# Kernel optimization log

Measured on AMD Instinct MI355X. Metric: run time of the kernel, lower is better.

## Reference

```python
import jax, jax.numpy as jnp
import numpy as np

EMBED = 1024
HEADS = 16
HEAD_DIM = EMBED // HEADS
BASE = 10000.0


def _rope_cos_sin(seq_len, dim, dtype):
    inv_freq = 1.0 / (BASE ** (jnp.arange(0, dim, 2, dtype=jnp.float32) / dim))
    t = jnp.arange(seq_len, dtype=jnp.float32)
    freqs = jnp.einsum('i,j->ij', t, inv_freq)           # [S, dim/2]
    emb = jnp.concatenate([freqs, freqs], axis=-1)        # [S, dim]
    return jnp.cos(emb).astype(dtype), jnp.sin(emb).astype(dtype)


def _rotate_half(x):
    d = x.shape[-1] // 2
    return jnp.concatenate([-x[..., d:], x[..., :d]], axis=-1)


def setup_inputs() -> dict:
    key = jax.random.key(0)
    ks = jax.random.split(key, 7)
    B, S = 2, 2048
    scale = 0.02
    return {
        'query': jax.random.normal(ks[0], (B, S, EMBED), jnp.float32),
        'key': jax.random.normal(ks[1], (B, S, EMBED), jnp.float32),
        'value': jax.random.normal(ks[2], (B, S, EMBED), jnp.float32),
        'Wq': jax.random.normal(ks[3], (EMBED, EMBED), jnp.float32) * scale,
        'Wk': jax.random.normal(ks[4], (EMBED, EMBED), jnp.float32) * scale,
        'Wv': jax.random.normal(ks[5], (EMBED, EMBED), jnp.float32) * scale,
        'Wo': jax.random.normal(ks[6], (EMBED, EMBED), jnp.float32) * scale,
    }


def reference(query, key, value, Wq, Wk, Wv, Wo):
    B, Sq, _ = query.shape
    Sk = key.shape[1]
    # projections (bias-free Linear: x @ W^T; W sampled so use x @ W directly)
    q = (query @ Wq).reshape(B, Sq, HEADS, HEAD_DIM).transpose(0, 2, 1, 3)  # [B,H,Sq,Dh]
    k = (key @ Wk).reshape(B, Sk, HEADS, HEAD_DIM).transpose(0, 2, 1, 3)
    v = (value @ Wv).reshape(B, Sk, HEADS, HEAD_DIM).transpose(0, 2, 1, 3)
    # RoPE applied to q and k per-position
    cos_q, sin_q = _rope_cos_sin(Sq, HEAD_DIM, q.dtype)  # [Sq,Dh]
    cos_k, sin_k = _rope_cos_sin(Sk, HEAD_DIM, k.dtype)
    q = q * cos_q[None, None] + _rotate_half(q) * sin_q[None, None]
    k = k * cos_k[None, None] + _rotate_half(k) * sin_k[None, None]
    scores = jnp.einsum('bhqd,bhkd->bhqk', q, k) / jnp.sqrt(jnp.asarray(HEAD_DIM, q.dtype))
    probs = jax.nn.softmax(scores, axis=-1)
    out = jnp.einsum('bhqk,bhkd->bhqd', probs, v)
    out = out.transpose(0, 2, 1, 3).reshape(B, Sq, EMBED)
    return out @ Wo
```

## Files before the change

kernel.cpp:

```cpp
#include <hip/hip_runtime.h>
#include <hip/hip_bf16.h>


typedef unsigned short u16;
typedef unsigned int u32;
typedef __attribute__((ext_vector_type(8))) short short8;
typedef __attribute__((ext_vector_type(4))) float f32x4;

#define MFMA16(a, b, c) __builtin_amdgcn_mfma_f32_16x16x32_bf16((a), (b), (c), 0, 0, 0)

typedef __attribute__((address_space(3))) u16 lds_u16;
typedef __attribute__((address_space(1))) const u16 glb_u16;

__device__ __forceinline__ void gload16(const u16* g, u16* l) {
    __builtin_amdgcn_global_load_lds((glb_u16*)g, (lds_u16*)l, 16, 0, 0);
}

__device__ __forceinline__ u16 f2bf(float f) {
    __hip_bfloat16 h = __float2bfloat16(f);
    return *reinterpret_cast<u16*>(&h);
}
__device__ __forceinline__ float bf2f(u16 b) {
    __hip_bfloat16 h;
    *reinterpret_cast<u16*>(&h) = b;
    return __bfloat162float(h);
}

__global__ __launch_bounds__(256) void conv_x(const float* __restrict__ q,
                                              const float* __restrict__ k,
                                              const float* __restrict__ v,
                                              u16* __restrict__ X3) {
    int z = blockIdx.y;
    const float* src = (z == 0) ? q : (z == 1) ? k : v;
    int i = (blockIdx.x * 256 + threadIdx.x) * 4;
    float4 f = *reinterpret_cast<const float4*>(src + i);
    ushort4 o;
    o.x = f2bf(f.x); o.y = f2bf(f.y); o.z = f2bf(f.z); o.w = f2bf(f.w);
    *reinterpret_cast<ushort4*>(X3 + (size_t)z * 4194304 + i) = o;
}

__global__ __launch_bounds__(256) void transpose_w(const float* __restrict__ w0,
                                                   const float* __restrict__ w1,
                                                   const float* __restrict__ w2,
                                                   const float* __restrict__ w3,
                                                   u16* __restrict__ WT) {
    __shared__ float t[32][33];
    const float* Ws[4] = {w0, w1, w2, w3};
    const float* W = Ws[blockIdx.z];
    int n0 = blockIdx.x * 32, k0 = blockIdx.y * 32;
    int tx = threadIdx.x, ty = threadIdx.y;
    for (int r = 0; r < 4; r++) {
        int kk = ty + r * 8;
        t[kk][tx] = W[(k0 + kk) * 1024 + n0 + tx];
    }
    __syncthreads();
    u16* out = WT + (size_t)blockIdx.z * 1048576;
    for (int r = 0; r < 4; r++) {
        int nn = ty + r * 8;
        out[(n0 + nn) * 1024 + k0 + tx] = f2bf(t[tx][nn]);
    }
}

template <typename OutT>
__global__ __launch_bounds__(256) void gemm_bt(const u16* __restrict__ A,
                                               const u16* __restrict__ Bt,
                                               OutT* __restrict__ C,
                                               int M, int N, int K) {
    int z = blockIdx.z;
    A  += (size_t)z * M * K;
    Bt += (size_t)z * N * K;
    C  += (size_t)z * M * N;
    int m0 = blockIdx.y * 128, n0 = blockIdx.x * 128;
    __shared__ u16 As[128 * 32];
    __shared__ u16 Bs[128 * 32];
    int tid = threadIdx.x;
    int wave = tid >> 6, lane = tid & 63, quad = lane >> 4, l16 = lane & 15;
    int wm = (wave >> 1) * 64, wn = (wave & 1) * 64;
    f32x4 acc[4][4];
    for (int i = 0; i < 4; i++)
        for (int j = 0; j < 4; j++)
            for (int r = 0; r < 4; r++) acc[i][j][r] = 0.f;

    for (int k0 = 0; k0 < K; k0 += 32) {
        __syncthreads();
        for (int c = 0; c < 2; c++) {
            int e = (tid + c * 256) * 8;
            int row = e >> 5, col = e & 31;
            gload16(&A[(size_t)(m0 + row) * K + k0 + col], &As[e]);
            gload16(&Bt[(size_t)(n0 + row) * K + k0 + col], &Bs[e]);
        }
        __syncthreads();
        short8 af[4], bfr[4];
        for (int i = 0; i < 4; i++)
            af[i] = *reinterpret_cast<const short8*>(&As[(wm + i * 16 + l16) * 32 + quad * 8]);
        for (int j = 0; j < 4; j++)
            bfr[j] = *reinterpret_cast<const short8*>(&Bs[(wn + j * 16 + l16) * 32 + quad * 8]);
        for (int i = 0; i < 4; i++)
            for (int j = 0; j < 4; j++)
                acc[i][j] = MFMA16(af[i], bfr[j], acc[i][j]);
    }

    for (int i = 0; i < 4; i++) {
        for (int r = 0; r < 4; r++) {
            int m = m0 + wm + i * 16 + quad * 4 + r;
            for (int j = 0; j < 4; j++) {
                int n = n0 + wn + j * 16 + l16;
                float v = acc[i][j][r];
                if constexpr (sizeof(OutT) == 2)
                    C[(size_t)m * N + n] = (OutT)f2bf(v);
                else
                    C[(size_t)m * N + n] = (OutT)v;
            }
        }
    }
}

__global__ __launch_bounds__(256) void rope_pack(const u16* __restrict__ QKV,
                                                 u16* __restrict__ Qp,
                                                 u16* __restrict__ Kp) {
    int z = blockIdx.y;
    int gid = blockIdx.x * 256 + threadIdx.x;
    int row = gid >> 5;
    int d = gid & 31;
    int b = row >> 15;
    int rem = row & 32767;
    int s = rem >> 4;
    int h = rem & 15;
    const u16* src = QKV + (size_t)z * 4194304 + (size_t)row * 64;
    float x1 = bf2f(src[d]);
    float x2 = bf2f(src[d + 32]);
    float inv = powf(10000.f, -(float)d / 32.f);
    float fr = (float)s * inv;
    float c = cosf(fr), sn = sinf(fr);
    float o1 = x1 * c - x2 * sn;
    float o2 = x2 * c + x1 * sn;
    if (z == 0) { o1 *= 0.125f; o2 *= 0.125f; }
    u16* dst = ((z == 0) ? Qp : Kp) + (((size_t)(b * 16 + h)) * 2048 + s) * 64;
    dst[d] = f2bf(o1);
    dst[d + 32] = f2bf(o2);
}

__global__ __launch_bounds__(256) void v_transpose(const u16* __restrict__ Vsrc,
                                                   u16* __restrict__ Vt) {
    __shared__ u16 t[64 * 72];
    int s0 = blockIdx.x * 64, bh = blockIdx.y;
    int b = bh >> 4, h = bh & 15;
    int tid = threadIdx.x;
    int srow = tid >> 3, scol = (tid & 7) * 8;
    for (int c = 0; c < 2; c++) {
        int s = srow + c * 32;
        *reinterpret_cast<int4*>(&t[s * 72 + scol]) =
            *reinterpret_cast<const int4*>(&Vsrc[((size_t)(b * 2048 + s0 + s)) * 1024 + h * 64 + scol]);
    }
    __syncthreads();
    for (int c = 0; c < 2; c++) {
        int d = srow + c * 32;
        short8 o;
        for (int j = 0; j < 8; j++) o[j] = (short)t[(scol + j) * 72 + d];
        *reinterpret_cast<short8*>(&Vt[(size_t)bh * 131072 + (size_t)d * 2048 + s0 + scol]) = o;
    }
}

__global__ __launch_bounds__(256) void flash_attn(const u16* __restrict__ Qp,
                                                  const u16* __restrict__ Kp,
                                                  const u16* __restrict__ Vt_g,
                                                  u16* __restrict__ attn) {
    int q0 = blockIdx.x * 64, bh = blockIdx.y;
    const u16* Q = Qp + (size_t)bh * 131072;
    const u16* K = Kp + (size_t)bh * 131072;
    const u16* Vt = Vt_g + (size_t)bh * 131072;
    __shared__ u16 Ks[64 * 72];
    __shared__ u16 Vs[64 * 72];
    __shared__ u16 Ps[64 * 72];
    int tid = threadIdx.x, wave = tid >> 6, lane = tid & 63;
    int quad = lane >> 4, l16 = lane & 15;
    int srow = tid >> 3, scol = (tid & 7) * 8;

    short8 qf[2];
    for (int kk = 0; kk < 2; kk++)
        qf[kk] = *reinterpret_cast<const short8*>(
            &Q[(size_t)(q0 + wave * 16 + l16) * 64 + kk * 32 + quad * 8]);

    float psum = 0.f;
    f32x4 Oacc[4];
    for (int dt = 0; dt < 4; dt++)
        for (int r = 0; r < 4; r++) Oacc[dt][r] = 0.f;

    for (int kv0 = 0; kv0 < 2048; kv0 += 64) {
        __syncthreads();
        for (int c = 0; c < 2; c++) {
            int row = srow + c * 32;
            *reinterpret_cast<int4*>(&Ks[row * 72 + scol]) =
                *reinterpret_cast<const int4*>(&K[(size_t)(kv0 + row) * 64 + scol]);
            *reinterpret_cast<int4*>(&Vs[row * 72 + scol]) =
                *reinterpret_cast<const int4*>(&Vt[(size_t)row * 2048 + kv0 + scol]);
        }
        __syncthreads();

        f32x4 st[4];
        for (int nt = 0; nt < 4; nt++)
            for (int r = 0; r < 4; r++) st[nt][r] = 0.f;
        for (int kk = 0; kk < 2; kk++)
            for (int nt = 0; nt < 4; nt++) {
                short8 af = *reinterpret_cast<const short8*>(
                    &Ks[(nt * 16 + l16) * 72 + kk * 32 + quad * 8]);
                st[nt] = MFMA16(af, qf[kk], st[nt]);
            }

        for (int nt = 0; nt < 4; nt++) {
            float p0 = __expf(st[nt][0]);
            float p1 = __expf(st[nt][1]);
            float p2 = __expf(st[nt][2]);
            float p3 = __expf(st[nt][3]);
            psum += (p0 + p1) + (p2 + p3);
            uint2 w;
            w.x = (u32)f2bf(p0) | ((u32)f2bf(p1) << 16);
            w.y = (u32)f2bf(p2) | ((u32)f2bf(p3) << 16);
            *reinterpret_cast<uint2*>(&Ps[(wave * 16 + l16) * 72 + nt * 16 + quad * 4]) = w;
        }

        for (int kk = 0; kk < 2; kk++) {
            short8 pa = *reinterpret_cast<const short8*>(
                &Ps[(wave * 16 + l16) * 72 + kk * 32 + quad * 8]);
            for (int dt = 0; dt < 4; dt++) {
                short8 bv = *reinterpret_cast<const short8*>(
                    &Vs[(dt * 16 + l16) * 72 + kk * 32 + quad * 8]);
                Oacc[dt] = MFMA16(pa, bv, Oacc[dt]);
            }
        }
    }

    psum += __shfl_xor(psum, 16);
    psum += __shfl_xor(psum, 32);
    float linv[4];
    for (int r = 0; r < 4; r++)
        linv[r] = 1.f / __shfl(psum, quad * 4 + r);

    int b = bh >> 4, h = bh & 15;
    for (int dt = 0; dt < 4; dt++)
        for (int r = 0; r < 4; r++) {
            int s = q0 + wave * 16 + quad * 4 + r;
            attn[((size_t)(b * 2048 + s)) * 1024 + h * 64 + dt * 16 + l16] =
                f2bf(Oacc[dt][r] * linv[r]);
        }
}

extern "C" void kernel_launch(void* const* d_in, const int* in_sizes, int n_in,
                              void* d_out, int out_size, void* d_ws, size_t ws_size,
                              hipStream_t stream) {
    const float* q  = (const float*)d_in[0];
    const float* k  = (const float*)d_in[1];
    const float* v  = (const float*)d_in[2];
    const float* wq = (const float*)d_in[3];
    const float* wk = (const float*)d_in[4];
    const float* wv = (const float*)d_in[5];
    const float* wo = (const float*)d_in[6];

    u16* ws = (u16*)d_ws;
    u16* WT  = ws;
    u16* X3  = ws + (size_t)4 * 1048576;
    u16* QKV = X3 + (size_t)3 * 4194304;
    u16* Qp   = X3;
    u16* Kp   = X3 + (size_t)1 * 4194304;
    u16* Vt_g = X3 + (size_t)2 * 4194304;
    u16* attn = QKV;

    conv_x<<<dim3(4096, 3), 256, 0, stream>>>(q, k, v, X3);
    transpose_w<<<dim3(32, 32, 4), dim3(32, 8), 0, stream>>>(wq, wk, wv, wo, WT);
    gemm_bt<u16><<<dim3(8, 32, 3), 256, 0, stream>>>(X3, WT, QKV, 4096, 1024, 1024);
    rope_pack<<<dim3(8192, 2), 256, 0, stream>>>(QKV, Qp, Kp);
    v_transpose<<<dim3(32, 32), 256, 0, stream>>>(QKV + (size_t)2 * 4194304, Vt_g);
    flash_attn<<<dim3(32, 32), 256, 0, stream>>>(Qp, Kp, Vt_g, attn);
    gemm_bt<float><<<dim3(8, 32, 1), 256, 0, stream>>>(
        attn, WT + (size_t)3 * 1048576, (float*)d_out, 4096, 1024, 1024);
}
```

Before: 285.9 us.

## Fuse RoPE into QKV GEMM epilogue and double query rows per attention block

The QKV projection epilogue now applies RoPE (from a precomputed cos/sin table) and the query scale, and writes head-major Q/K/V directly, so the separate rope_pack pass and its extra round trip through memory are gone. The RoPE table is built by a small kernel in the output buffer before the final GEMM overwrites it. Flash attention now processes 128 query rows per block (two 16-row groups per wave), so each K/V tile loaded into LDS is reused by twice as many queries, at the cost of more registers and half as many blocks. The epilogue stores are scattered 2-byte writes with table lookups, which may add some write inefficiency.

```diff
diff --git a/kernel.cpp b/kernel.cpp
--- a/kernel.cpp
+++ b/kernel.cpp
@@ -19,11 +19,6 @@
 __device__ __forceinline__ u16 f2bf(float f) {
     __hip_bfloat16 h = __float2bfloat16(f);
     return *reinterpret_cast<u16*>(&h);
-}
-__device__ __forceinline__ float bf2f(u16 b) {
-    __hip_bfloat16 h;
-    *reinterpret_cast<u16*>(&h) = b;
-    return __bfloat162float(h);
 }
 
 __global__ __launch_bounds__(256) void conv_x(const float* __restrict__ q,
@@ -61,15 +56,24 @@
     }
 }
 
-template <typename OutT>
-__global__ __launch_bounds__(256) void gemm_bt(const u16* __restrict__ A,
-                                               const u16* __restrict__ Bt,
-                                               OutT* __restrict__ C,
-                                               int M, int N, int K) {
+__global__ __launch_bounds__(256) void rope_table(float2* __restrict__ tab) {
+    int gid = blockIdx.x * 256 + threadIdx.x;
+    int s = gid >> 5, d = gid & 31;
+    float inv = powf(10000.f, -(float)d / 32.f);
+    float fr = (float)s * inv;
+    tab[gid] = make_float2(cosf(fr), sinf(fr));
+}
+
+__global__ __launch_bounds__(256) void gemm_qkv(const u16* __restrict__ Aall,
+                                                const u16* __restrict__ WT,
+                                                u16* __restrict__ Qp,
+                                                u16* __restrict__ Kp,
+                                                u16* __restrict__ Vsd,
+                                                const float2* __restrict__ tab) {
     int z = blockIdx.z;
-    A  += (size_t)z * M * K;
-    Bt += (size_t)z * N * K;
-    C  += (size_t)z * M * N;
+    const u16* A  = Aall + (size_t)z * 4194304;
+    const u16* Bt = WT + (size_t)z * 1048576;
+    const int K = 1024;
     int m0 = blockIdx.y * 128, n0 = blockIdx.x * 128;
     __shared__ u16 As[128 * 32];
     __shared__ u16 Bs[128 * 32];
@@ -100,57 +104,89 @@
                 acc[i][j] = MFMA16(af[i], bfr[j], acc[i][j]);
     }
 
-    for (int i = 0; i < 4; i++) {
+    int h = (n0 + wn) >> 6;
+    if (z == 2) {
+        for (int i = 0; i < 4; i++)
+            for (int r = 0; r < 4; r++) {
+                int m = m0 + wm + i * 16 + quad * 4 + r;
+                int b = m >> 11, s = m & 2047;
+                u16* row = Vsd + (((size_t)(b * 16 + h)) * 2048 + s) * 64;
+                for (int j = 0; j < 4; j++)
+                    row[j * 16 + l16] = f2bf(acc[i][j][r]);
+            }
+    } else {
+        u16* base = (z == 0) ? Qp : Kp;
+        float scale = (z == 0) ? 0.125f : 1.f;
+        for (int i = 0; i < 4; i++)
+            for (int r = 0; r < 4; r++) {
+                int m = m0 + wm + i * 16 + quad * 4 + r;
+                int b = m >> 11, s = m & 2047;
+                u16* row = base + (((size_t)(b * 16 + h)) * 2048 + s) * 64;
+                for (int j = 0; j < 2; j++) {
+                    int d = j * 16 + l16;
+                    float2 cs = tab[s * 32 + d];
+                    float x1 = acc[i][j][r] * scale;
+                    float x2 = acc[i][j + 2][r] * scale;
+                    row[d]      = f2bf(x1 * cs.x - x2 * cs.y);
+                    row[d + 32] = f2bf(x2 * cs.x + x1 * cs.y);
+                }
+            }
+    }
+}
+
+__global__ __launch_bounds__(256) void gemm_bt_f32(const u16* __restrict__ A,
+                                                   const u16* __restrict__ Bt,
+                                                   float* __restrict__ C,
+                                                   int M, int N, int K) {
+    int m0 = blockIdx.y * 128, n0 = blockIdx.x * 128;
+    __shared__ u16 As[128 * 32];
+    __shared__ u16 Bs[128 * 32];
+    int tid = threadIdx.x;
+    int wave = tid >> 6, lane = tid & 63, quad = lane >> 4, l16 = lane & 15;
+    int wm = (wave >> 1) * 64, wn = (wave & 1) * 64;
+    f32x4 acc[4][4];
+    for (int i = 0; i < 4; i++)
+        for (int j = 0; j < 4; j++)
+            for (int r = 0; r < 4; r++) acc[i][j][r] = 0.f;
+
+    for (int k0 = 0; k0 < K; k0 += 32) {
+        __syncthreads();
+        for (int c = 0; c < 2; c++) {
+            int e = (tid + c * 256) * 8;
+            int row = e >> 5, col = e & 31;
+            gload16(&A[(size_t)(m0 + row) * K + k0 + col], &As[e]);
+            gload16(&Bt[(size_t)(n0 + row) * K + k0 + col], &Bs[e]);
+        }
+        __syncthreads();
+        short8 af[4], bfr[4];
+        for (int i = 0; i < 4; i++)
+            af[i] = *reinterpret_cast<const short8*>(&As[(wm + i * 16 + l16) * 32 + quad * 8]);
+        for (int j = 0; j < 4; j++)
+            bfr[j] = *reinterpret_cast<const short8*>(&Bs[(wn + j * 16 + l16) * 32 + quad * 8]);
+        for (int i = 0; i < 4; i++)
+            for (int j = 0; j < 4; j++)
+                acc[i][j] = MFMA16(af[i], bfr[j], acc[i][j]);
+    }
+
+    for (int i = 0; i < 4; i++)
         for (int r = 0; r < 4; r++) {
             int m = m0 + wm + i * 16 + quad * 4 + r;
-            for (int j = 0; j < 4; j++) {
-                int n = n0 + wn + j * 16 + l16;
-                float v = acc[i][j][r];
-                if constexpr (sizeof(OutT) == 2)
-                    C[(size_t)m * N + n] = (OutT)f2bf(v);
-                else
-                    C[(size_t)m * N + n] = (OutT)v;
-            }
-        }
-    }
-}
-
-__global__ __launch_bounds__(256) void rope_pack(const u16* __restrict__ QKV,
-                                                 u16* __restrict__ Qp,
-                                                 u16* __restrict__ Kp) {
-    int z = blockIdx.y;
-    int gid = blockIdx.x * 256 + threadIdx.x;
-    int row = gid >> 5;
-    int d = gid & 31;
-    int b = row >> 15;
-    int rem = row & 32767;
-    int s = rem >> 4;
-    int h = rem & 15;
-    const u16* src = QKV + (size_t)z * 4194304 + (size_t)row * 64;
-    float x1 = bf2f(src[d]);
-    float x2 = bf2f(src[d + 32]);
-    float inv = powf(10000.f, -(float)d / 32.f);
-    float fr = (float)s * inv;
-    float c = cosf(fr), sn = sinf(fr);
-    float o1 = x1 * c - x2 * sn;
-    float o2 = x2 * c + x1 * sn;
-    if (z == 0) { o1 *= 0.125f; o2 *= 0.125f; }
-    u16* dst = ((z == 0) ? Qp : Kp) + (((size_t)(b * 16 + h)) * 2048 + s) * 64;
-    dst[d] = f2bf(o1);
-    dst[d + 32] = f2bf(o2);
-}
-
-__global__ __launch_bounds__(256) void v_transpose(const u16* __restrict__ Vsrc,
+            for (int j = 0; j < 4; j++)
+                C[(size_t)m * N + n0 + wn + j * 16 + l16] = acc[i][j][r];
+        }
+}
+
+__global__ __launch_bounds__(256) void v_transpose(const u16* __restrict__ Vsd,
                                                    u16* __restrict__ Vt) {
     __shared__ u16 t[64 * 72];
     int s0 = blockIdx.x * 64, bh = blockIdx.y;
-    int b = bh >> 4, h = bh & 15;
+    const u16* src = Vsd + (size_t)bh * 131072;
     int tid = threadIdx.x;
     int srow = tid >> 3, scol = (tid & 7) * 8;
     for (int c = 0; c < 2; c++) {
         int s = srow + c * 32;
         *reinterpret_cast<int4*>(&t[s * 72 + scol]) =
-            *reinterpret_cast<const int4*>(&Vsrc[((size_t)(b * 2048 + s0 + s)) * 1024 + h * 64 + scol]);
+            *reinterpret_cast<const int4*>(&src[(size_t)(s0 + s) * 64 + scol]);
     }
     __syncthreads();
     for (int c = 0; c < 2; c++) {
@@ -165,26 +201,28 @@
                                                   const u16* __restrict__ Kp,
                                                   const u16* __restrict__ Vt_g,
                                                   u16* __restrict__ attn) {
-    int q0 = blockIdx.x * 64, bh = blockIdx.y;
+    int q0 = blockIdx.x * 128, bh = blockIdx.y;
     const u16* Q = Qp + (size_t)bh * 131072;
     const u16* K = Kp + (size_t)bh * 131072;
     const u16* Vt = Vt_g + (size_t)bh * 131072;
     __shared__ u16 Ks[64 * 72];
     __shared__ u16 Vs[64 * 72];
-    __shared__ u16 Ps[64 * 72];
+    __shared__ u16 Ps[128 * 72];
     int tid = threadIdx.x, wave = tid >> 6, lane = tid & 63;
     int quad = lane >> 4, l16 = lane & 15;
     int srow = tid >> 3, scol = (tid & 7) * 8;
 
-    short8 qf[2];
-    for (int kk = 0; kk < 2; kk++)
-        qf[kk] = *reinterpret_cast<const short8*>(
-            &Q[(size_t)(q0 + wave * 16 + l16) * 64 + kk * 32 + quad * 8]);
-
-    float psum = 0.f;
-    f32x4 Oacc[4];
-    for (int dt = 0; dt < 4; dt++)
-        for (int r = 0; r < 4; r++) Oacc[dt][r] = 0.f;
+    short8 qf[2][2];
+    for (int g = 0; g < 2; g++)
+        for (int kk = 0; kk < 2; kk++)
+            qf[g][kk] = *reinterpret_cast<const short8*>(
+                &Q[(size_t)(q0 + wave * 32 + g * 16 + l16) * 64 + kk * 32 + quad * 8]);
+
+    float psum[2] = {0.f, 0.f};
+    f32x4 Oacc[2][4];
+    for (int g = 0; g < 2; g++)
+        for (int dt = 0; dt < 4; dt++)
+            for (int r = 0; r < 4; r++) Oacc[g][dt][r] = 0.f;
 
     for (int kv0 = 0; kv0 < 2048; kv0 += 64) {
         __syncthreads();
@@ -197,52 +235,61 @@
         }
         __syncthreads();
 
-        f32x4 st[4];
-        for (int nt = 0; nt < 4; nt++)
-            for (int r = 0; r < 4; r++) st[nt][r] = 0.f;
+        f32x4 st[2][4];
+        for (int g = 0; g < 2; g++)
+            for (int nt = 0; nt < 4; nt++)
+                for (int r = 0; r < 4; r++) st[g][nt][r] = 0.f;
         for (int kk = 0; kk < 2; kk++)
             for (int nt = 0; nt < 4; nt++) {
                 short8 af = *reinterpret_cast<const short8*>(
                     &Ks[(nt * 16 + l16) * 72 + kk * 32 + quad * 8]);
-                st[nt] = MFMA16(af, qf[kk], st[nt]);
-            }
-
-        for (int nt = 0; nt < 4; nt++) {
-            float p0 = __expf(st[nt][0]);
-            float p1 = __expf(st[nt][1]);
-            float p2 = __expf(st[nt][2]);
-            float p3 = __expf(st[nt][3]);
-            psum += (p0 + p1) + (p2 + p3);
-            uint2 w;
-            w.x = (u32)f2bf(p0) | ((u32)f2bf(p1) << 16);
-            w.y = (u32)f2bf(p2) | ((u32)f2bf(p3) << 16);
-            *reinterpret_cast<uint2*>(&Ps[(wave * 16 + l16) * 72 + nt * 16 + quad * 4]) = w;
-        }
+                for (int g = 0; g < 2; g++)
+                    st[g][nt] = MFMA16(af, qf[g][kk], st[g][nt]);
+            }
+
+        for (int g = 0; g < 2; g++)
+            for (int nt = 0; nt < 4; nt++) {
+                float p0 = __expf(st[g][nt][0]);
+                float p1 = __expf(st[g][nt][1]);
+                float p2 = __expf(st[g][nt][2]);
+                float p3 = __expf(st[g][nt][3]);
+                psum[g] += (p0 + p1) + (p2 + p3);
+                uint2 w;
+                w.x = (u32)f2bf(p0) | ((u32)f2bf(p1) << 16);
+                w.y = (u32)f2bf(p2) | ((u32)f2bf(p3) << 16);
+                *reinterpret_cast<uint2*>(
+                    &Ps[(wave * 32 + g * 16 + l16) * 72 + nt * 16 + quad * 4]) = w;
+            }
 
         for (int kk = 0; kk < 2; kk++) {
-            short8 pa = *reinterpret_cast<const short8*>(
-                &Ps[(wave * 16 + l16) * 72 + kk * 32 + quad * 8]);
+            short8 pa[2];
+            for (int g = 0; g < 2; g++)
+                pa[g] = *reinterpret_cast<const short8*>(
+                    &Ps[(wave * 32 + g * 16 + l16) * 72 + kk * 32 + quad * 8]);
             for (int dt = 0; dt < 4; dt++) {
                 short8 bv = *reinterpret_cast<const short8*>(
                     &Vs[(dt * 16 + l16) * 72 + kk * 32 + quad * 8]);
-                Oacc[dt] = MFMA16(pa, bv, Oacc[dt]);
-            }
-        }
-    }
-
-    psum += __shfl_xor(psum, 16);
-    psum += __shfl_xor(psum, 32);
-    float linv[4];
-    for (int r = 0; r < 4; r++)
-        linv[r] = 1.f / __shfl(psum, quad * 4 + r);
+                for (int g = 0; g < 2; g++)
+                    Oacc[g][dt] = MFMA16(pa[g], bv, Oacc[g][dt]);
+            }
+        }
+    }
 
     int b = bh >> 4, h = bh & 15;
-    for (int dt = 0; dt < 4; dt++)
-        for (int r = 0; r < 4; r++) {
-            int s = q0 + wave * 16 + quad * 4 + r;
-            attn[((size_t)(b * 2048 + s)) * 1024 + h * 64 + dt * 16 + l16] =
-                f2bf(Oacc[dt][r] * linv[r]);
-        }
+    for (int g = 0; g < 2; g++) {
+        float ps = psum[g];
+        ps += __shfl_xor(ps, 16);
+        ps += __shfl_xor(ps, 32);
+        float linv[4];
+        for (int r = 0; r < 4; r++)
+            linv[r] = 1.f / __shfl(ps, quad * 4 + r);
+        for (int dt = 0; dt < 4; dt++)
+            for (int r = 0; r < 4; r++) {
+                int s = q0 + wave * 32 + g * 16 + quad * 4 + r;
+                attn[((size_t)(b * 2048 + s)) * 1024 + h * 64 + dt * 16 + l16] =
+                    f2bf(Oacc[g][dt][r] * linv[r]);
+            }
+    }
 }
 
 extern "C" void kernel_launch(void* const* d_in, const int* in_sizes, int n_in,
@@ -260,17 +307,19 @@
     u16* WT  = ws;
     u16* X3  = ws + (size_t)4 * 1048576;
     u16* QKV = X3 + (size_t)3 * 4194304;
-    u16* Qp   = X3;
-    u16* Kp   = X3 + (size_t)1 * 4194304;
+    u16* Qp  = QKV;
+    u16* Kp  = QKV + (size_t)1 * 4194304;
+    u16* Vsd = QKV + (size_t)2 * 4194304;
+    u16* attn = X3;
     u16* Vt_g = X3 + (size_t)2 * 4194304;
-    u16* attn = QKV;
+    float2* tab = (float2*)d_out;
 
     conv_x<<<dim3(4096, 3), 256, 0, stream>>>(q, k, v, X3);
     transpose_w<<<dim3(32, 32, 4), dim3(32, 8), 0, stream>>>(wq, wk, wv, wo, WT);
-    gemm_bt<u16><<<dim3(8, 32, 3), 256, 0, stream>>>(X3, WT, QKV, 4096, 1024, 1024);
-    rope_pack<<<dim3(8192, 2), 256, 0, stream>>>(QKV, Qp, Kp);
-    v_transpose<<<dim3(32, 32), 256, 0, stream>>>(QKV + (size_t)2 * 4194304, Vt_g);
-    flash_attn<<<dim3(32, 32), 256, 0, stream>>>(Qp, Kp, Vt_g, attn);
-    gemm_bt<float><<<dim3(8, 32, 1), 256, 0, stream>>>(
+    rope_table<<<256, 256, 0, stream>>>(tab);
+    gemm_qkv<<<dim3(8, 32, 3), 256, 0, stream>>>(X3, WT, Qp, Kp, Vsd, tab);
+    v_transpose<<<dim3(32, 32), 256, 0, stream>>>(Vsd, Vt_g);
+    flash_attn<<<dim3(16, 32), 256, 0, stream>>>(Qp, Kp, Vt_g, attn);
+    gemm_bt_f32<<<dim3(8, 32, 1), 256, 0, stream>>>(
         attn, WT + (size_t)3 * 1048576, (float*)d_out, 4096, 1024, 1024);
 }
```

Result: faster. 275.9 us (-3.5%).
